# Kernel optimization log

Measured on AMD Instinct MI355X. Metric: run time of the kernel, lower is better.

The kernel has to match this reference:

```python
import jax, jax.numpy as jnp
import numpy as np

B, TQ, M, D, H, F, L = 4, 512, 512, 1024, 16, 4096, 6
S = D // H
R = TQ + M  # relative-attention length = memory + query
CUTOFFS = [20000, 40000, 200000]
PROJ_FACTOR = 4
LN_EPS = 1e-6
NEG_INF = -1e9


def setup_inputs() -> dict:
    key = jax.random.key(0)
    ks = iter(jax.random.split(key, 64))

    def w(shape, scale=0.02):
        return jax.random.normal(next(ks), shape, jnp.float32) * scale

    inp = {}
    inp['token_ids'] = jax.random.randint(next(ks), (B, TQ), 0, CUTOFFS[-1])
    inp['memories'] = w((L, B, M, D))
    starts = [0] + CUTOFFS
    pf = 1
    for i in range(len(CUTOFFS)):
        psize = max(1, D // pf)
        inp['emb_table%d' % i] = w((starts[i + 1] - starts[i], psize))
        inp['emb_proj%d' % i] = w((psize, D))
        pf *= PROJ_FACTOR
    inp['wq'] = w((L, D, H, S)); inp['wk'] = w((L, D, H, S))
    inp['wv'] = w((L, D, H, S)); inp['wr'] = w((L, D, H, S))
    inp['wo'] = w((L, H, S, D))
    inp['content_bias'] = w((L, H, S)); inp['position_bias'] = w((L, H, S))
    inp['ln1_scale'] = jnp.ones((L, D)); inp['ln1_bias'] = jnp.zeros((L, D))
    inp['ln2_scale'] = jnp.ones((L, D)); inp['ln2_bias'] = jnp.zeros((L, D))
    inp['ffn_w1'] = w((L, D, F)); inp['ffn_b1'] = jnp.zeros((L, F))
    inp['ffn_w2'] = w((L, F, D)); inp['ffn_b2'] = jnp.zeros((L, D))
    return inp


def layernorm(x, scale, bias):
    mu = jnp.mean(x, axis=-1, keepdims=True)
    var = jnp.var(x, axis=-1, keepdims=True)
    return (x - mu) * jax.lax.rsqrt(var + LN_EPS) * scale + bias


def rel_shift(x):
    # x: [B, H, Q, R] -> shifted so position j aligns with relative distance
    b, h, q, r = x.shape
    x = jnp.pad(x, ((0, 0), (0, 0), (0, 0), (1, 0)))
    x = x.reshape(b, h, r + 1, q)[:, :, 1:, :]
    return x.reshape(b, h, q, r)


def positional_encoding(r_len, d):
    pos = jnp.arange(r_len - 1, -1, -1, dtype=jnp.float32)  # r_len-1 ... 0
    inv_freq = 1.0 / (10000.0 ** (jnp.arange(0, d, 2, dtype=jnp.float32) / d))
    sinusoid = pos[:, None] * inv_freq[None, :]
    return jnp.concatenate([jnp.sin(sinusoid), jnp.cos(sinusoid)], axis=-1)


def adaptive_embed(ids, tables, projs):
    # jit-friendly version of AdaptiveEmbedding.compute_embeddings:
    # gather per-cluster, project up to D, combine via masks.
    d = projs[0].shape[-1]
    y = jnp.zeros(ids.shape + (d,), jnp.float32)
    starts = [0] + CUTOFFS
    for tab, proj, lo, hi in zip(tables, projs, starts[:-1], starts[1:]):
        mask = (ids >= lo) & (ids < hi)
        idx = jnp.clip(ids - lo, 0, tab.shape[0] - 1)
        emb = jnp.einsum('btp,pd->btd', tab[idx], proj)
        y = y + jnp.where(mask[..., None], emb, 0.0)
    return y * (d ** 0.5)


def transformer_xl(token_ids, memories, emb_tables, emb_projs, wq, wk, wv, wr,
                   wo, content_bias, position_bias, ln1_scale, ln1_bias,
                   ln2_scale, ln2_bias, ffn_w1, ffn_b1, ffn_w2, ffn_b2):
    x = adaptive_embed(token_ids, emb_tables, emb_projs)  # [B, TQ, D]
    pe = positional_encoding(R, D)                        # [R, D]
    q_idx = jnp.arange(TQ)[:, None]
    r_idx = jnp.arange(R)[None, :]
    future = r_idx > q_idx + M                            # [TQ, R], True=masked
    scale = 1.0 / np.sqrt(S).astype(np.float32)
    for l in range(L):
        q = jnp.einsum('btd,dhs->bths', x, wq[l])
        kv_in = jnp.concatenate([memories[l], x], axis=1)  # [B, R, D]
        k = jnp.einsum('brd,dhs->brhs', kv_in, wk[l])
        v = jnp.einsum('brd,dhs->brhs', kv_in, wv[l])
        r = jnp.einsum('rd,dhs->rhs', pe, wr[l])
        ac = jnp.einsum('bqhs,brhs->bhqr', q + content_bias[l], k)
        bd = rel_shift(jnp.einsum('bqhs,rhs->bhqr', q + position_bias[l], r))
        scores = (ac + bd) * scale
        scores = jnp.where(future[None, None], NEG_INF, scores)
        attn = jax.nn.softmax(scores, axis=-1)
        ctx = jnp.einsum('bhqr,brhs->bqhs', attn, v)
        out = jnp.einsum('bqhs,hsd->bqd', ctx, wo[l])
        x = layernorm(x + out, ln1_scale[l], ln1_bias[l])
        h = jax.nn.relu(jnp.einsum('btd,df->btf', x, ffn_w1[l]) + ffn_b1[l])
        h = jnp.einsum('btf,fd->btd', h, ffn_w2[l]) + ffn_b2[l]
        x = layernorm(x + h, ln2_scale[l], ln2_bias[l])
    return x


def reference(token_ids, memories, emb_table0, emb_proj0, emb_table1,
              emb_proj1, emb_table2, emb_proj2, wq, wk, wv, wr, wo,
              content_bias, position_bias, ln1_scale, ln1_bias, ln2_scale,
              ln2_bias, ffn_w1, ffn_b1, ffn_w2, ffn_b2):
    return transformer_xl(
        token_ids, memories,
        [emb_table0, emb_table1, emb_table2],
        [emb_proj0, emb_proj1, emb_proj2],
        wq, wk, wv, wr, wo, content_bias, position_bias,
        ln1_scale, ln1_bias, ln2_scale, ln2_bias,
        ffn_w1, ffn_b1, ffn_w2, ffn_b2)
```

## Files before the change

### kernel.cpp

```cpp
#include <hip/hip_runtime.h>


#define Bc 4
#define TQc 512
#define Mc 512
#define Dc 1024
#define Hc 16
#define Sc 64
#define Fc 4096
#define Lc 6
#define Rc 1024
#define KCAT 1344
#define DDc ((size_t)Dc * Dc)
#define NEG_INF_F (-1e9f)

typedef unsigned short ushortT;
typedef __attribute__((ext_vector_type(8))) short bfrag;
typedef __attribute__((ext_vector_type(4))) float facc;

__device__ inline ushortT f2bf(float f) {
    unsigned int u = __builtin_bit_cast(unsigned int, f);
    u = (u + 0x7FFFu + ((u >> 16) & 1u)) >> 16;
    return (ushortT)u;
}

#define CP16(gp, lp)                                                        \
    __builtin_amdgcn_global_load_lds(                                       \
        (const __attribute__((address_space(1))) unsigned int*)(gp),        \
        (__attribute__((address_space(3))) unsigned int*)(lp), 16, 0, 0)

__device__ inline bfrag lds_frag(const ushortT* lds, int row, int cg) {
    int c = cg ^ (row & 7);
    return *reinterpret_cast<const bfrag*>(
        reinterpret_cast<const char*>(lds) + row * 128 + c * 16);
}

template<int BM, int BN, int OUTM, bool BIAS, bool RELU, bool DUALQ,
         bool KVSRC = false, bool KVOUT = false>
__device__ __forceinline__ void mgemm_body(
    char* smemraw,
    const ushortT* __restrict__ A, const ushortT* __restrict__ A2,
    const ushortT* __restrict__ Bt,
    const float* __restrict__ bias, const float* __restrict__ bias2,
    float* __restrict__ Cf, ushortT* __restrict__ Cb, ushortT* __restrict__ Cb2,
    int K, int lda, int ldb, int ldc, float oscale, int bx, int by) {
    constexpr int WTM = BM / 2, WTN = BN / 2;
    constexpr int FM = WTM / 16, FN = WTN / 16;
    ushortT* sAb = (ushortT*)smemraw;
    ushortT* sBb = sAb + 2 * BM * 64;
    int tid = threadIdx.x;
    int wave = tid >> 6, lane = tid & 63;
    int r16 = lane & 15, kgrp = lane >> 4;
    int wr = wave >> 1, wc = wave & 1;

    int row0 = by * BM, col0 = bx * BN;
    facc acc[FM][FN] = {};

    auto STAGE = [&](int buf, int k0) {
        #pragma unroll
        for (int it = 0; it < BM / 32; ++it) {
            int s = it * 256 + tid;
            int row = s >> 3, c = s & 7;
            int cs = c ^ (row & 7);
            const char* g;
            if constexpr (KVSRC) {
                int arow = row0 + row;
                int bq = arow >> 10;
                int r = arow & 1023;
                if (r < Mc)
                    g = (const char*)(A + ((size_t)bq * Mc + r) * lda + k0) + cs * 16;
                else
                    g = (const char*)(A2 + ((size_t)bq * TQc + (r - Mc)) * lda + k0) + cs * 16;
            } else {
                g = (const char*)(A + (size_t)(row0 + row) * lda + k0) + cs * 16;
            }
            CP16(g, (char*)(sAb + buf * BM * 64) + s * 16);
        }
        #pragma unroll
        for (int it = 0; it < BN / 32; ++it) {
            int s = it * 256 + tid;
            int row = s >> 3, c = s & 7;
            int cs = c ^ (row & 7);
            CP16((const char*)(Bt + (size_t)(col0 + row) * ldb + k0) + cs * 16,
                 (char*)(sBb + buf * BN * 64) + s * 16);
        }
    };

    STAGE(0, 0);
    __syncthreads();
    int nk = K >> 6;
    for (int t = 0; t < nk; ++t) {
        int cur = t & 1;
        if (t + 1 < nk) STAGE(cur ^ 1, (t + 1) << 6);
        #pragma unroll
        for (int ks = 0; ks < 2; ++ks) {
            bfrag af[FM], bf[FN];
            #pragma unroll
            for (int mi = 0; mi < FM; ++mi)
                af[mi] = lds_frag(sAb + cur * BM * 64, wr * WTM + mi * 16 + r16, ks * 4 + kgrp);
            #pragma unroll
            for (int ni = 0; ni < FN; ++ni)
                bf[ni] = lds_frag(sBb + cur * BN * 64, wc * WTN + ni * 16 + r16, ks * 4 + kgrp);
            #pragma unroll
            for (int mi = 0; mi < FM; ++mi)
                #pragma unroll
                for (int ni = 0; ni < FN; ++ni)
                    acc[mi][ni] = __builtin_amdgcn_mfma_f32_16x16x32_bf16(
                        af[mi], bf[ni], acc[mi][ni], 0, 0, 0);
        }
        __syncthreads();
    }

    if constexpr (KVOUT) {
        if (col0 >= 1024) {
            ushortT* sT = sAb;
            int b = row0 >> 10, r0l = row0 & 1023;
            int h0 = (col0 - 1024) >> 6;
            #pragma unroll
            for (int p = 0; p < 2; ++p) {
                __syncthreads();
                if (wc == p) {
                    #pragma unroll
                    for (int mi = 0; mi < FM; ++mi)
                        #pragma unroll
                        for (int ni = 0; ni < FN; ++ni) {
                            int srow = ni * 16 + r16;
                            int cbase = wr * 64 + mi * 16 + kgrp * 4;
                            short4 s4;
                            s4.x = (short)f2bf(acc[mi][ni][0]);
                            s4.y = (short)f2bf(acc[mi][ni][1]);
                            s4.z = (short)f2bf(acc[mi][ni][2]);
                            s4.w = (short)f2bf(acc[mi][ni][3]);
                            *(short4*)(sT + srow * 132 + cbase) = s4;
                        }
                }
                __syncthreads();
                int h = h0 + p;
                #pragma unroll
                for (int it = 0; it < 4; ++it) {
                    int srow = it * 16 + (tid >> 4);
                    int rch = (tid & 15) * 8;
                    short4 lo = *(short4*)(sT + srow * 132 + rch);
                    short4 hi = *(short4*)(sT + srow * 132 + rch + 4);
                    ushortT* dst = Cb2 + ((size_t)((b * 16 + h) * 64 + srow)) * Rc
                                   + r0l + rch;
                    *(short4*)dst = lo;
                    *(short4*)(dst + 4) = hi;
                }
            }
            return;
        }
    }

    #pragma unroll
    for (int mi = 0; mi < FM; ++mi) {
        #pragma unroll
        for (int ni = 0; ni < FN; ++ni) {
            int gcol = col0 + wc * WTN + ni * 16 + r16;
            float bv = 0.0f, bv2 = 0.0f;
            if (BIAS || DUALQ) bv = bias[gcol];
            if (DUALQ) bv2 = bias2[gcol];
            #pragma unroll
            for (int j = 0; j < 4; ++j) {
                int grow = row0 + wr * WTM + mi * 16 + kgrp * 4 + j;
                float v = acc[mi][ni][j];
                if constexpr (DUALQ) {
                    Cb [(size_t)grow * ldc + gcol] = f2bf((v + bv) * oscale);
                    Cb2[(size_t)grow * ldc + gcol] = f2bf((v + bv2) * oscale);
                } else if constexpr (OUTM == 2) {
                    v *= oscale;
                    Cf[(size_t)grow * ldc + gcol] = v;
                    Cb[(size_t)grow * ldc + gcol] = f2bf(v);
                } else {
                    if (BIAS) v += bv;
                    if (RELU) v = fmaxf(v, 0.0f);
                    if constexpr (OUTM == 0)
                        Cf[(size_t)grow * ldc + gcol] = v;
                    else if constexpr (OUTM == 3)
                        unsafeAtomicAdd(&Cf[(size_t)grow * ldc + gcol], v);
                    else
                        Cb[(size_t)grow * ldc + gcol] = f2bf(v);
                }
            }
        }
    }
}

template<int BM, int BN, int OUTM, bool BIAS, bool RELU, bool DUALQ,
         bool KVSRC = false, bool KVOUT = false>
__global__ __launch_bounds__(256) void mgemm(
    const ushortT* __restrict__ A, const ushortT* __restrict__ A2,
    const ushortT* __restrict__ Bt,
    const float* __restrict__ bias, const float* __restrict__ bias2,
    float* __restrict__ Cf, ushortT* __restrict__ Cb, ushortT* __restrict__ Cb2,
    int K, int lda, int ldb, int ldc,
    long long sA1, long long sB1, long long sC1, float oscale) {
    __shared__ char smem[2 * (BM + BN) * 64 * 2];
    int z = blockIdx.z;
    A  += (long long)z * sA1;
    Bt += (long long)z * sB1;
    long long coff = (long long)z * sC1;
    if (OUTM != 1) Cf += coff;
    if (OUTM != 0 || DUALQ) Cb += coff;
    mgemm_body<BM, BN, OUTM, BIAS, RELU, DUALQ, KVSRC, KVOUT>(
        smem, A, A2, Bt, bias, bias2, Cf, Cb, Cb2,
        K, lda, ldb, ldc, oscale, blockIdx.x, blockIdx.y);
}

__global__ __launch_bounds__(256) void qkv_gemm(
    const ushortT* __restrict__ xb, const ushortT* __restrict__ membl,
    const ushortT* __restrict__ wqTl, const ushortT* __restrict__ wkvTl,
    const float* __restrict__ cbl, const float* __restrict__ pbl,
    ushortT* __restrict__ qc, ushortT* __restrict__ qp,
    ushortT* __restrict__ kbuf, ushortT* __restrict__ vT) {
    __shared__ char smem[2 * (128 + 128) * 64 * 2];
    if (blockIdx.z == 0)
        mgemm_body<64, 64, 1, false, false, true, false, false>(
            smem, xb, nullptr, wqTl, cbl, pbl, nullptr, qc, qp,
            Dc, Dc, Dc, Dc, 0.125f, blockIdx.x, blockIdx.y);
    else
        mgemm_body<128, 128, 1, false, false, false, true, true>(
            smem, membl, xb, wkvTl, nullptr, nullptr, nullptr, kbuf, vT,
            Dc, Dc, Dc, 1024, 1.0f, blockIdx.x, blockIdx.y);
}

__global__ __launch_bounds__(256) void fused_attn(
    const ushortT* __restrict__ qc, const ushortT* __restrict__ qp,
    const ushortT* __restrict__ kb, const ushortT* __restrict__ vT,
    const ushortT* __restrict__ rp, ushortT* __restrict__ ctx) {
    int n_id = (int)(blockIdx.y << 3) | (int)blockIdx.x;
    int b0 = n_id & 1, b7 = (n_id >> 7) & 1, b8 = (n_id >> 8) & 1;
    int u = (b7 << 1) | b0;
    int qt = (b0 ^ b8) ? (7 - u) : u;
    int bh = (n_id >> 1) & 63;
    int b = bh >> 4, h = bh & 15;
    int q0 = qt * 64;
    __shared__ __align__(16) char smem[73728];
    ushortT* sQc = (ushortT*)smem;
    ushortT* sQp = (ushortT*)(smem + 8192);
    float*   sBD = (float*)smem;
    ushortT* sK  = (ushortT*)(smem + 16384);
    ushortT* sV  = (ushortT*)(smem + 32768);
    ushortT* sR  = (ushortT*)(smem + 49152);
    int tid = threadIdx.x;
    int lane = tid & 63, wq = tid >> 6;
    int r16 = lane & 15, kgrp = lane >> 4;
    char* sPb = smem + wq * 4096;

    const ushortT* qcb = qc + (size_t)(b * TQc + q0) * Dc + h * 64;
    const ushortT* qpb = qp + (size_t)(b * TQc + q0) * Dc + h * 64;
    const ushortT* kbb = kb + (size_t)b * Rc * 1024 + h * 64;
    const ushortT* vTb = vT + (size_t)bh * 64 * Rc;
    const ushortT* rpb = rp + h * 64;
    int rrbase0 = 448 - q0;
    int iters = qt + 9;

    #pragma unroll
    for (int it = 0; it < 2; ++it) {
        int s = it * 256 + tid;
        int row = s >> 3, c = s & 7;
        int cs = c ^ (row & 7);
        CP16((const char*)(qcb + (size_t)row * Dc) + cs * 16, (char*)sQc + s * 16);
        CP16((const char*)(qpb + (size_t)row * Dc) + cs * 16, (char*)sQp + s * 16);
        CP16((const char*)(kbb + (size_t)row * 1024) + cs * 16, (char*)sK + s * 16);
        CP16((const char*)(vTb + (size_t)row * Rc) + cs * 16, (char*)sV + s * 16);
    }
    #pragma unroll
    for (int hR = 0; hR < 2; ++hR) {
        #pragma unroll
        for (int it = 0; it < 2; ++it) {
            int s = it * 256 + tid;
            int row = s >> 3, c = s & 7;
            int cs = c ^ (row & 7);
            int gr = rrbase0 + hR * 64 + row;
            gr = gr > 1023 ? 1023 : gr;
            CP16((const char*)(rpb + (size_t)gr * Dc) + cs * 16,
                 (char*)sR + hR * 8192 + s * 16);
        }
    }
    __syncthreads();

    bfrag hqc[2], hqp[2];
    #pragma unroll
    for (int ks = 0; ks < 2; ++ks) {
        hqc[ks] = lds_frag(sQc, wq * 16 + r16, ks * 4 + kgrp);
        hqp[ks] = lds_frag(sQp, wq * 16 + r16, ks * 4 + kgrp);
    }
    __syncthreads();

    facc accO[4] = {};
    float m[4] = {-1e30f, -1e30f, -1e30f, -1e30f};
    float lsum[4] = {};

    for (int itj = 0; itj < iters; ++itj) {
        int j0 = itj * 64;
        __syncthreads();
        int cur = itj & 1;
        int ph0 = itj % 3, ph1 = (itj + 1) % 3;

        if (itj + 1 < iters) {
            int jn = j0 + 64;
            #pragma unroll
            for (int it2 = 0; it2 < 2; ++it2) {
                int s = it2 * 256 + tid;
                int row = s >> 3, c = s & 7;
                int cs = c ^ (row & 7);
                CP16((const char*)(kbb + (size_t)(jn + row) * 1024) + cs * 16,
                     (char*)sK + (cur ^ 1) * 8192 + s * 16);
                CP16((const char*)(vTb + (size_t)row * Rc + jn) + cs * 16,
                     (char*)sV + (cur ^ 1) * 8192 + s * 16);
            }
        }
        if (itj + 2 <= iters) {
            int L = itj + 2;
            int p2 = L % 3;
            #pragma unroll
            for (int it2 = 0; it2 < 2; ++it2) {
                int s = it2 * 256 + tid;
                int row = s >> 3, c = s & 7;
                int cs = c ^ (row & 7);
                int gr = rrbase0 + L * 64 + row;
                gr = gr > 1023 ? 1023 : gr;
                CP16((const char*)(rpb + (size_t)gr * Dc) + cs * 16,
                     (char*)sR + p2 * 8192 + s * 16);
            }
        }

        facc aac[4] = {};
        facc abd[5] = {};
        __builtin_amdgcn_s_setprio(1);
        #pragma unroll
        for (int ks = 0; ks < 2; ++ks) {
            #pragma unroll
            for (int n = 0; n < 4; ++n) {
                bfrag bk = lds_frag(sK + cur * 4096, n * 16 + r16, ks * 4 + kgrp);
                aac[n] = __builtin_amdgcn_mfma_f32_16x16x32_bf16(hqc[ks], bk, aac[n], 0, 0, 0);
            }
            #pragma unroll
            for (int n = 0; n < 5; ++n) {
                int t = 3 - wq + n;
                int p = (t >> 2) ? ph1 : ph0;
                bfrag br = lds_frag(sR + p * 4096, (t & 3) * 16 + r16, ks * 4 + kgrp);
                abd[n] = __builtin_amdgcn_mfma_f32_16x16x32_bf16(hqp[ks], br, abd[n], 0, 0, 0);
            }
        }
        __builtin_amdgcn_s_setprio(0);
        #pragma unroll
        for (int n = 0; n < 5; ++n) {
            int rl = (3 - wq + n) * 16 + r16;
            #pragma unroll
            for (int jj = 0; jj < 4; ++jj) {
                int ql = wq * 16 + kgrp * 4 + jj;
                int jl = rl + ql - 63;
                if (jl >= 0 && jl < 64)
                    sBD[ql * 64 + (jl ^ (((ql >> 2) & 1) << 4))] = abd[n][jj];
            }
        }

        bool lastit = (itj == iters - 1);
        float P[4][4];
        #pragma unroll
        for (int jj = 0; jj < 4; ++jj) {
            int ql = wq * 16 + kgrp * 4 + jj;
            int swz = ((ql >> 2) & 1) << 4;
            float sv[4];
            #pragma unroll
            for (int n = 0; n < 4; ++n) {
                int jl = n * 16 + r16;
                sv[n] = aac[n][jj] + sBD[ql * 64 + (jl ^ swz)];
            }
            if (lastit) {
                int qg = q0 + ql;
                #pragma unroll
                for (int n = 0; n < 4; ++n) {
                    int jg = j0 + n * 16 + r16;
                    if (jg > qg + Mc) sv[n] = NEG_INF_F;
                }
            }
            float mx = fmaxf(fmaxf(sv[0], sv[1]), fmaxf(sv[2], sv[3]));
            mx = fmaxf(mx, __shfl_xor(mx, 1));
            mx = fmaxf(mx, __shfl_xor(mx, 2));
            mx = fmaxf(mx, __shfl_xor(mx, 4));
            mx = fmaxf(mx, __shfl_xor(mx, 8));
            float mnew = fmaxf(m[jj], mx);
            float corr = __expf(m[jj] - mnew);
            m[jj] = mnew;
            float rs = 0.0f;
            #pragma unroll
            for (int n = 0; n < 4; ++n) {
                float p = __expf(sv[n] - mnew);
                P[n][jj] = p;
                rs += p;
            }
            rs += __shfl_xor(rs, 1);
            rs += __shfl_xor(rs, 2);
            rs += __shfl_xor(rs, 4);
            rs += __shfl_xor(rs, 8);
            lsum[jj] = lsum[jj] * corr + rs;
            #pragma unroll
            for (int n = 0; n < 4; ++n) accO[n][jj] *= corr;
        }
        #pragma unroll
        for (int jj = 0; jj < 4; ++jj) {
            int row = wq * 16 + kgrp * 4 + jj;
            #pragma unroll
            for (int n = 0; n < 4; ++n) {
                int col = n * 16 + r16;
                int boff = (row & 15) * 128 + (((col >> 3) ^ (row & 7)) * 16) + (col & 7) * 2;
                *(ushortT*)(sPb + boff) = f2bf(P[n][jj]);
            }
        }
        __builtin_amdgcn_s_setprio(1);
        #pragma unroll
        for (int ks = 0; ks < 2; ++ks) {
            bfrag pa = *(const bfrag*)(sPb + r16 * 128 + (((ks * 4 + kgrp) ^ (r16 & 7)) * 16));
            #pragma unroll
            for (int n = 0; n < 4; ++n) {
                bfrag bv = lds_frag(sV + cur * 4096, n * 16 + r16, ks * 4 + kgrp);
                accO[n] = __builtin_amdgcn_mfma_f32_16x16x32_bf16(pa, bv, accO[n], 0, 0, 0);
            }
        }
        __builtin_amdgcn_s_setprio(0);
    }
    #pragma unroll
    for (int jj = 0; jj < 4; ++jj) {
        int qg = q0 + wq * 16 + kgrp * 4 + jj;
        float inv = 1.0f / lsum[jj];
        #pragma unroll
        for (int n = 0; n < 4; ++n) {
            int col = n * 16 + r16;
            ctx[(size_t)(b * TQc + qg) * Dc + h * 64 + col] = f2bf(accO[n][jj] * inv);
        }
    }
}

__global__ __launch_bounds__(256) void tr_f32_bf16(
    const float* __restrict__ in, ushortT* __restrict__ out, int R0, int C0,
    int ldout, int coff, long long inZ, long long outZ) {
    in += (long long)blockIdx.z * inZ;
    out += (long long)blockIdx.z * outZ;
    __shared__ float t[32][33];
    int tx = threadIdx.x & 31, ty = threadIdx.x >> 5;
    int c0 = blockIdx.x * 32, r0 = blockIdx.y * 32;
    #pragma unroll
    for (int i = 0; i < 4; ++i)
        t[ty + i * 8][tx] = in[(size_t)(r0 + ty + i * 8) * C0 + c0 + tx];
    __syncthreads();
    int c = threadIdx.x >> 3, rq = (threadIdx.x & 7) << 2;
    short4 s4;
    s4.x = (short)f2bf(t[rq + 0][c]);
    s4.y = (short)f2bf(t[rq + 1][c]);
    s4.z = (short)f2bf(t[rq + 2][c]);
    s4.w = (short)f2bf(t[rq + 3][c]);
    *(short4*)(out + (size_t)(c0 + c) * ldout + coff + r0 + rq) = s4;
}

__global__ __launch_bounds__(256) void tr_dxd5(
    const float* __restrict__ wr, const float* __restrict__ wq,
    const float* __restrict__ wk, const float* __restrict__ wv,
    const float* __restrict__ wo,
    ushortT* __restrict__ wrT, ushortT* __restrict__ wqT,
    ushortT* __restrict__ wkvT, ushortT* __restrict__ woT) {
    int sel = blockIdx.z / Lc, l = blockIdx.z % Lc;
    const float* in; ushortT* out;
    if (sel == 0)      { in = wr + l * DDc; out = wrT + l * DDc; }
    else if (sel == 1) { in = wq + l * DDc; out = wqT + l * DDc; }
    else if (sel == 2) { in = wk + l * DDc; out = wkvT + l * 2 * DDc; }
    else if (sel == 3) { in = wv + l * DDc; out = wkvT + l * 2 * DDc + DDc; }
    else               { in = wo + l * DDc; out = woT + l * DDc; }
    __shared__ float t[32][33];
    int tx = threadIdx.x & 31, ty = threadIdx.x >> 5;
    int c0 = blockIdx.x * 32, r0 = blockIdx.y * 32;
    #pragma unroll
    for (int i = 0; i < 4; ++i)
        t[ty + i * 8][tx] = in[(size_t)(r0 + ty + i * 8) * Dc + c0 + tx];
    __syncthreads();
    int c = threadIdx.x >> 3, rq = (threadIdx.x & 7) << 2;
    short4 s4;
    s4.x = (short)f2bf(t[rq + 0][c]);
    s4.y = (short)f2bf(t[rq + 1][c]);
    s4.z = (short)f2bf(t[rq + 2][c]);
    s4.w = (short)f2bf(t[rq + 3][c]);
    *(short4*)(out + (size_t)(c0 + c) * Dc + r0 + rq) = s4;
}

__global__ __launch_bounds__(256) void pos_enc_kernel(ushortT* __restrict__ pe) {
    int idx = blockIdx.x * 256 + threadIdx.x;
    int r = idx >> 10;
    int d = idx & 1023;
    float pos = (float)(Rc - 1 - r);
    int i = (d < 512) ? d : (d - 512);
    float inv_freq = 1.0f / powf(10000.0f, (2.0f * (float)i) / 1024.0f);
    float arg = pos * inv_freq;
    pe[idx] = f2bf((d < 512) ? sinf(arg) : cosf(arg));
}

__global__ __launch_bounds__(256) void gather_embed(
    const int* __restrict__ ids,
    const float* __restrict__ t0, const float* __restrict__ t1,
    const float* __restrict__ t2, ushortT* __restrict__ gcat) {
    int token = blockIdx.x;
    int id = ids[token];
    ushortT* row = gcat + (size_t)token * KCAT;
    short4 z4 = {0, 0, 0, 0};
    for (int t = threadIdx.x; t < KCAT / 4; t += 256)
        reinterpret_cast<short4*>(row)[t] = z4;
    __syncthreads();
    const float* tab; int psize, lo, o;
    if (id < 20000)      { tab = t0; psize = 1024; lo = 0;     o = 0; }
    else if (id < 40000) { tab = t1; psize = 256;  lo = 20000; o = 1024; }
    else                 { tab = t2; psize = 64;   lo = 40000; o = 1280; }
    const float* src = tab + (size_t)(id - lo) * psize;
    for (int p4 = threadIdx.x; p4 < psize / 4; p4 += 256) {
        float4 v = reinterpret_cast<const float4*>(src)[p4];
        short4 s4;
        s4.x = (short)f2bf(v.x); s4.y = (short)f2bf(v.y);
        s4.z = (short)f2bf(v.z); s4.w = (short)f2bf(v.w);
        reinterpret_cast<short4*>(row + o)[p4] = s4;
    }
}

__global__ __launch_bounds__(256) void cast_f32_bf16(
    const float* __restrict__ in, ushortT* __restrict__ o) {
    size_t i8 = ((size_t)blockIdx.x * 256 + threadIdx.x) * 8;
    const float4* m4 = (const float4*)(in + i8);
    float4 a = m4[0], c = m4[1];
    int4 p;
    p.x = (int)f2bf(a.x) | ((int)f2bf(a.y) << 16);
    p.y = (int)f2bf(a.z) | ((int)f2bf(a.w) << 16);
    p.z = (int)f2bf(c.x) | ((int)f2bf(c.y) << 16);
    p.w = (int)f2bf(c.z) | ((int)f2bf(c.w) << 16);
    *(int4*)(o + i8) = p;
}

template<int NP, bool CBIAS, bool ZR0 = false>
__global__ __launch_bounds__(256) void add_ln_kernel(
    const float* __restrict__ xin, const float* __restrict__ r0,
    const float* __restrict__ r1, const float* __restrict__ r2,
    const float* __restrict__ r3, const float* __restrict__ cbias,
    const float* __restrict__ scale, const float* __restrict__ bias,
    float* __restrict__ dst, ushortT* __restrict__ dstb,
    float* __restrict__ r0z) {
    int row = blockIdx.x * 4 + (threadIdx.x >> 6);
    int lane = threadIdx.x & 63;
    const float4* xr = (const float4*)(xin + (size_t)row * Dc);
    const float4* p0 = (const float4*)(r0 + (size_t)row * Dc);
    const float4* p1 = nullptr; const float4* p2 = nullptr; const float4* p3 = nullptr;
    if constexpr (NP > 1) p1 = (const float4*)(r1 + (size_t)row * Dc);
    if constexpr (NP > 2) p2 = (const float4*)(r2 + (size_t)row * Dc);
    if constexpr (NP > 3) p3 = (const float4*)(r3 + (size_t)row * Dc);
    const float4* cb4 = CBIAS ? (const float4*)cbias : nullptr;
    float4 v[4];
    float s = 0.0f, s2 = 0.0f;
    #pragma unroll
    for (int rep = 0; rep < 4; ++rep) {
        int idx = rep * 64 + lane;
        float4 a = xr[idx];
        float4 b = p0[idx];
        a.x += b.x; a.y += b.y; a.z += b.z; a.w += b.w;
        if constexpr (NP > 1) {
            float4 c1 = p1[idx];
            a.x += c1.x; a.y += c1.y; a.z += c1.z; a.w += c1.w;
        }
        if constexpr (NP > 2) {
            float4 c2 = p2[idx];
            a.x += c2.x; a.y += c2.y; a.z += c2.z; a.w += c2.w;
        }
        if constexpr (NP > 3) {
            float4 c3 = p3[idx];
            a.x += c3.x; a.y += c3.y; a.z += c3.z; a.w += c3.w;
        }
        if constexpr (CBIAS) {
            float4 cbv = cb4[idx];
            a.x += cbv.x; a.y += cbv.y; a.z += cbv.z; a.w += cbv.w;
        }
        v[rep] = a;
        s += a.x + a.y + a.z + a.w;
        s2 += a.x * a.x + a.y * a.y + a.z * a.z + a.w * a.w;
    }
    if constexpr (ZR0) {
        float4 zz = {0.0f, 0.0f, 0.0f, 0.0f};
        float4* z4 = (float4*)(r0z + (size_t)row * Dc);
        #pragma unroll
        for (int rep = 0; rep < 4; ++rep) z4[rep * 64 + lane] = zz;
    }
    #pragma unroll
    for (int o = 1; o < 64; o <<= 1) {
        s += __shfl_xor(s, o);
        s2 += __shfl_xor(s2, o);
    }
    float mean = s * (1.0f / Dc);
    float var = s2 * (1.0f / Dc) - mean * mean;
    float rstd = rsqrtf(var + 1e-6f);
    float4* d4 = (float4*)(dst + (size_t)row * Dc);
    short4* db4 = (short4*)(dstb + (size_t)row * Dc);
    const float4* sc4 = (const float4*)scale;
    const float4* bi4 = (const float4*)bias;
    #pragma unroll
    for (int rep = 0; rep < 4; ++rep) {
        int idx = rep * 64 + lane;
        float4 scv = sc4[idx], biv = bi4[idx];
        float4 a = v[rep];
        float4 o;
        o.x = (a.x - mean) * rstd * scv.x + biv.x;
        o.y = (a.y - mean) * rstd * scv.y + biv.y;
        o.z = (a.z - mean) * rstd * scv.z + biv.z;
        o.w = (a.w - mean) * rstd * scv.w + biv.w;
        d4[idx] = o;
        short4 ob;
        ob.x = (short)f2bf(o.x); ob.y = (short)f2bf(o.y);
        ob.z = (short)f2bf(o.z); ob.w = (short)f2bf(o.w);
        db4[idx] = ob;
    }
}

extern "C" void kernel_launch(void* const* d_in, const int* in_sizes, int n_in,
                              void* d_out, int out_size, void* d_ws, size_t ws_size,
                              hipStream_t stream) {
    const int*   token_ids = (const int*)d_in[0];
    const float* memories  = (const float*)d_in[1];
    const float* tab0 = (const float*)d_in[2];
    const float* prj0 = (const float*)d_in[3];
    const float* tab1 = (const float*)d_in[4];
    const float* prj1 = (const float*)d_in[5];
    const float* tab2 = (const float*)d_in[6];
    const float* prj2 = (const float*)d_in[7];
    const float* wq = (const float*)d_in[8];
    const float* wk = (const float*)d_in[9];
    const float* wv = (const float*)d_in[10];
    const float* wr = (const float*)d_in[11];
    const float* wo = (const float*)d_in[12];
    const float* cb = (const float*)d_in[13];
    const float* pb = (const float*)d_in[14];
    const float* ln1s = (const float*)d_in[15];
    const float* ln1b = (const float*)d_in[16];
    const float* ln2s = (const float*)d_in[17];
    const float* ln2b = (const float*)d_in[18];
    const float* w1 = (const float*)d_in[19];
    const float* b1 = (const float*)d_in[20];
    const float* w2 = (const float*)d_in[21];
    const float* b2 = (const float*)d_in[22];
    float* out = (float*)d_out;

    char* wsb = (char*)d_ws;
    size_t off = 0;
    auto alloc = [&](size_t bytes) {
        char* p = wsb + off;
        off += (bytes + 255) & ~(size_t)255;
        return p;
    };
    const size_t DD = DDc;
    const size_t TD = (size_t)Bc * TQc * Dc;
    const size_t DF = (size_t)Dc * Fc;
    ushortT* pe_b  = (ushortT*)alloc((size_t)Rc * Dc * 2);
    ushortT* wrT   = (ushortT*)alloc((size_t)Lc * DD * 2);
    ushortT* rpA   = (ushortT*)alloc((size_t)Lc * Rc * Dc * 2);
    ushortT* wqT   = (ushortT*)alloc((size_t)Lc * DD * 2);
    ushortT* wkvT  = (ushortT*)alloc((size_t)Lc * 2 * DD * 2);
    ushortT* woT   = (ushortT*)alloc((size_t)Lc * DD * 2);
    ushortT* w1T   = (ushortT*)alloc((size_t)Lc * DF * 2);
    ushortT* w2T   = (ushortT*)alloc((size_t)Lc * DF * 2);
    ushortT* memb  = (ushortT*)alloc((size_t)Lc * Bc * Mc * Dc * 2);
    ushortT* gcat  = (ushortT*)alloc((size_t)Bc * TQc * KCAT * 2);
    ushortT* WcatT = (ushortT*)alloc((size_t)Dc * KCAT * 2);
    float*   x     = (float*)alloc(TD * 4);
    ushortT* xb    = (ushortT*)alloc(TD * 2);
    ushortT* qc    = (ushortT*)alloc(TD * 2);
    ushortT* qp    = (ushortT*)alloc(TD * 2);
    ushortT* kbuf  = (ushortT*)alloc((size_t)Bc * Rc * 1024 * 2);
    ushortT* vT    = (ushortT*)alloc((size_t)Bc * Rc * Dc * 2);
    ushortT* ctxb  = (ushortT*)alloc(TD * 2);
    float*   obp   = (float*)alloc(TD * 4);
    ushortT* hb    = (ushortT*)alloc((size_t)Bc * TQc * Fc * 2);

    pos_enc_kernel<<<(Rc * Dc) / 256, 256, 0, stream>>>(pe_b);
    gather_embed<<<Bc * TQc, 256, 0, stream>>>(token_ids, tab0, tab1, tab2, gcat);
    tr_f32_bf16<<<dim3(32, 32), 256, 0, stream>>>(prj0, WcatT, 1024, 1024, KCAT, 0, 0, 0);
    tr_f32_bf16<<<dim3(32, 8), 256, 0, stream>>>(prj1, WcatT, 256, 1024, KCAT, 1024, 0, 0);
    tr_f32_bf16<<<dim3(32, 2), 256, 0, stream>>>(prj2, WcatT, 64, 1024, KCAT, 1280, 0, 0);
    mgemm<64, 64, 2, false, false, false><<<dim3(16, 32), 256, 0, stream>>>(
        gcat, nullptr, WcatT, nullptr, nullptr, x, xb, nullptr,
        KCAT, KCAT, KCAT, Dc, 0, 0, 0, 32.0f);

    tr_dxd5<<<dim3(32, 32, 5 * Lc), 256, 0, stream>>>(
        wr, wq, wk, wv, wo, wrT, wqT, wkvT, woT);
    tr_f32_bf16<<<dim3(128, 32, Lc), 256, 0, stream>>>(w1, w1T, Dc, Fc, Dc, 0, DF, DF);
    tr_f32_bf16<<<dim3(32, 128, Lc), 256, 0, stream>>>(w2, w2T, Fc, Dc, Fc, 0, DF, DF);
    cast_f32_bf16<<<(Lc * Bc * Mc * Dc) / (256 * 8), 256, 0, stream>>>(memories, memb);
    mgemm<64, 64, 1, false, false, false><<<dim3(16, 16, Lc), 256, 0, stream>>>(
        pe_b, nullptr, wrT, nullptr, nullptr, nullptr, rpA, nullptr,
        Dc, Dc, Dc, Dc, 0, (long long)DD, (long long)Rc * Dc, 1.0f);

    for (int l = 0; l < Lc; ++l) {
        const ushortT* membl = memb + (size_t)l * Bc * Mc * Dc;
        qkv_gemm<<<dim3(16, 32, 2), 256, 0, stream>>>(
            xb, membl, wqT + (size_t)l * DD, wkvT + (size_t)l * 2 * DD,
            cb + (size_t)l * Dc, pb + (size_t)l * Dc, qc, qp, kbuf, vT);

        fused_attn<<<dim3(8, 64), 256, 0, stream>>>(
            qc, qp, kbuf, vT, rpA + (size_t)l * Rc * Dc, ctxb);

        mgemm<64, 64, 0, false, false, false><<<dim3(16, 32), 256, 0, stream>>>(
            ctxb, nullptr, woT + (size_t)l * DD, nullptr, nullptr, obp, nullptr, nullptr,
            Dc, Dc, Dc, Dc, 0, 0, 0, 1.0f);
        add_ln_kernel<1, false, true><<<Bc * TQc / 4, 256, 0, stream>>>(
            x, obp, nullptr, nullptr, nullptr, nullptr,
            ln1s + (size_t)l * Dc, ln1b + (size_t)l * Dc, x, xb, obp);
        mgemm<128, 128, 1, true, true, false><<<dim3(32, 16), 256, 0, stream>>>(
            xb, nullptr, w1T + (size_t)l * DF, b1 + (size_t)l * Fc, nullptr,
            nullptr, hb, nullptr, Dc, Dc, Dc, Fc, 0, 0, 0, 1.0f);
        mgemm<128, 128, 3, false, false, false><<<dim3(8, 16, 4), 256, 0, stream>>>(
            hb, nullptr, w2T + (size_t)l * DF, nullptr, nullptr, obp, nullptr, nullptr,
            1024, Fc, Fc, Dc, 1024, 1024, 0, 1.0f);
        add_ln_kernel<1, true, false><<<Bc * TQc / 4, 256, 0, stream>>>(
            x, obp, nullptr, nullptr, nullptr, b2 + (size_t)l * Dc,
            ln2s + (size_t)l * Dc, ln2b + (size_t)l * Dc,
            (l == Lc - 1) ? out : x, xb, nullptr);
    }
}
```

Baseline: 1.249 ms.

## Retile projection GMEMMs, split-K output proj, lazy softmax rescale, simpler BD scatter

Several changes land together. The Q projection and the positional projection move to 128x64 tiles, and the KV half of qkv_gemm is spread over two z-slices. The output projection becomes a split-K atomic-accumulate GEMM over two K halves, so obp is zeroed once up front and zeroed again by the second add-LN. In attention, the BD scatter into shared memory is rewritten with precomputed bounds, and the online softmax only rescales when the running max grows by more than 8. The lazy rescale cuts exp and multiply work but lets unnormalised values grow, and the atomic split-K adds atomic traffic and nondeterministic summation order.

```diff
diff --git a/kernel.cpp b/kernel.cpp
--- a/kernel.cpp
+++ b/kernel.cpp
@@ -215,13 +215,14 @@
     ushortT* __restrict__ kbuf, ushortT* __restrict__ vT) {
     __shared__ char smem[2 * (128 + 128) * 64 * 2];
     if (blockIdx.z == 0)
-        mgemm_body<64, 64, 1, false, false, true, false, false>(
+        mgemm_body<128, 64, 1, false, false, true, false, false>(
             smem, xb, nullptr, wqTl, cbl, pbl, nullptr, qc, qp,
             Dc, Dc, Dc, Dc, 0.125f, blockIdx.x, blockIdx.y);
     else
         mgemm_body<128, 128, 1, false, false, false, true, true>(
             smem, membl, xb, wkvTl, nullptr, nullptr, nullptr, kbuf, vT,
-            Dc, Dc, Dc, 1024, 1.0f, blockIdx.x, blockIdx.y);
+            Dc, Dc, Dc, 1024, 1.0f, blockIdx.x,
+            blockIdx.y + ((int)blockIdx.z - 1) * 16);
 }
 
 __global__ __launch_bounds__(256) void fused_attn(
@@ -346,15 +347,17 @@
         }
         __builtin_amdgcn_s_setprio(0);
         #pragma unroll
-        for (int n = 0; n < 5; ++n) {
-            int rl = (3 - wq + n) * 16 + r16;
-            #pragma unroll
-            for (int jj = 0; jj < 4; ++jj) {
-                int ql = wq * 16 + kgrp * 4 + jj;
-                int jl = rl + ql - 63;
-                if (jl >= 0 && jl < 64)
-                    sBD[ql * 64 + (jl ^ (((ql >> 2) & 1) << 4))] = abd[n][jj];
-            }
+        for (int jj = 0; jj < 4; ++jj) {
+            int ql = wq * 16 + kgrp * 4 + jj;
+            int swz = ((ql >> 2) & 1) << 4;
+            int bj = r16 + kgrp * 4 + jj;
+            if (bj >= 15)
+                sBD[ql * 64 + ((bj - 15) ^ swz)] = abd[0][jj];
+            #pragma unroll
+            for (int n = 1; n < 4; ++n)
+                sBD[ql * 64 + ((n * 16 + bj - 15) ^ swz)] = abd[n][jj];
+            if (bj <= 14)
+                sBD[ql * 64 + ((bj + 49) ^ swz)] = abd[4][jj];
         }
 
         bool lastit = (itj == iters - 1);
@@ -382,13 +385,17 @@
             mx = fmaxf(mx, __shfl_xor(mx, 2));
             mx = fmaxf(mx, __shfl_xor(mx, 4));
             mx = fmaxf(mx, __shfl_xor(mx, 8));
-            float mnew = fmaxf(m[jj], mx);
-            float corr = __expf(m[jj] - mnew);
-            m[jj] = mnew;
+            if (mx > m[jj] + 8.0f) {
+                float corr = __expf(m[jj] - mx);
+                m[jj] = mx;
+                lsum[jj] *= corr;
+                #pragma unroll
+                for (int n = 0; n < 4; ++n) accO[n][jj] *= corr;
+            }
             float rs = 0.0f;
             #pragma unroll
             for (int n = 0; n < 4; ++n) {
-                float p = __expf(sv[n] - mnew);
+                float p = __expf(sv[n] - m[jj]);
                 P[n][jj] = p;
                 rs += p;
             }
@@ -396,9 +403,7 @@
             rs += __shfl_xor(rs, 2);
             rs += __shfl_xor(rs, 4);
             rs += __shfl_xor(rs, 8);
-            lsum[jj] = lsum[jj] * corr + rs;
-            #pragma unroll
-            for (int n = 0; n < 4; ++n) accO[n][jj] *= corr;
+            lsum[jj] += rs;
         }
         #pragma unroll
         for (int jj = 0; jj < 4; ++jj) {
@@ -531,6 +536,12 @@
     p.z = (int)f2bf(c.x) | ((int)f2bf(c.y) << 16);
     p.w = (int)f2bf(c.z) | ((int)f2bf(c.w) << 16);
     *(int4*)(o + i8) = p;
+}
+
+__global__ __launch_bounds__(256) void zero_f32(float* __restrict__ p) {
+    size_t i = ((size_t)blockIdx.x * 256 + threadIdx.x) * 4;
+    float4 z = {0.0f, 0.0f, 0.0f, 0.0f};
+    *(float4*)(p + i) = z;
 }
 
 template<int NP, bool CBIAS, bool ZR0 = false>
@@ -687,22 +698,23 @@
     tr_f32_bf16<<<dim3(128, 32, Lc), 256, 0, stream>>>(w1, w1T, Dc, Fc, Dc, 0, DF, DF);
     tr_f32_bf16<<<dim3(32, 128, Lc), 256, 0, stream>>>(w2, w2T, Fc, Dc, Fc, 0, DF, DF);
     cast_f32_bf16<<<(Lc * Bc * Mc * Dc) / (256 * 8), 256, 0, stream>>>(memories, memb);
-    mgemm<64, 64, 1, false, false, false><<<dim3(16, 16, Lc), 256, 0, stream>>>(
+    mgemm<128, 64, 1, false, false, false><<<dim3(16, 8, Lc), 256, 0, stream>>>(
         pe_b, nullptr, wrT, nullptr, nullptr, nullptr, rpA, nullptr,
         Dc, Dc, Dc, Dc, 0, (long long)DD, (long long)Rc * Dc, 1.0f);
+    zero_f32<<<(int)(TD / (256 * 4)), 256, 0, stream>>>(obp);
 
     for (int l = 0; l < Lc; ++l) {
         const ushortT* membl = memb + (size_t)l * Bc * Mc * Dc;
-        qkv_gemm<<<dim3(16, 32, 2), 256, 0, stream>>>(
+        qkv_gemm<<<dim3(16, 16, 3), 256, 0, stream>>>(
             xb, membl, wqT + (size_t)l * DD, wkvT + (size_t)l * 2 * DD,
             cb + (size_t)l * Dc, pb + (size_t)l * Dc, qc, qp, kbuf, vT);
 
         fused_attn<<<dim3(8, 64), 256, 0, stream>>>(
             qc, qp, kbuf, vT, rpA + (size_t)l * Rc * Dc, ctxb);
 
-        mgemm<64, 64, 0, false, false, false><<<dim3(16, 32), 256, 0, stream>>>(
+        mgemm<128, 64, 3, false, false, false><<<dim3(16, 16, 2), 256, 0, stream>>>(
             ctxb, nullptr, woT + (size_t)l * DD, nullptr, nullptr, obp, nullptr, nullptr,
-            Dc, Dc, Dc, Dc, 0, 0, 0, 1.0f);
+            512, Dc, Dc, Dc, 512, 512, 0, 1.0f);
         add_ln_kernel<1, false, true><<<Bc * TQc / 4, 256, 0, stream>>>(
             x, obp, nullptr, nullptr, nullptr, nullptr,
             ln1s + (size_t)l * Dc, ln1b + (size_t)l * Dc, x, xb, obp);
@@ -712,9 +724,9 @@
         mgemm<128, 128, 3, false, false, false><<<dim3(8, 16, 4), 256, 0, stream>>>(
             hb, nullptr, w2T + (size_t)l * DF, nullptr, nullptr, obp, nullptr, nullptr,
             1024, Fc, Fc, Dc, 1024, 1024, 0, 1.0f);
-        add_ln_kernel<1, true, false><<<Bc * TQc / 4, 256, 0, stream>>>(
+        add_ln_kernel<1, true, true><<<Bc * TQc / 4, 256, 0, stream>>>(
             x, obp, nullptr, nullptr, nullptr, b2 + (size_t)l * Dc,
             ln2s + (size_t)l * Dc, ln2b + (size_t)l * Dc,
-            (l == Lc - 1) ? out : x, xb, nullptr);
-    }
-}
+            (l == Lc - 1) ? out : x, xb, obp);
+    }
+}
```

New measurement: 1.292 ms. 1.03x slower.
